# Kernel tuning notes

Measured on AMD Instinct MI355X. Metric: run time of the kernel, lower is better.

Reference implementation:

```python
import jax, jax.numpy as jnp
import numpy as np

N_LEVELS = 16
N_FEATS = 2
LOG2_T = 19
BASE_RES = 16.0
FINEST_RES = 512.0
N_POINTS = 1_000_000
HASH_MASK = np.uint32((1 << LOG2_T) - 1)
PRIME1 = np.uint32(2654435761)  # second spatial-hash prime (first is 1)


def setup_inputs() -> dict:
    key = jax.random.key(0)
    k1, k2 = jax.random.split(key)
    x = jax.random.uniform(k1, (N_POINTS, 2), dtype=jnp.float32)
    # nn.init.uniform_(w, -1e-4, 1e-4) per level, stacked: [L, T, F]
    embeddings = (jax.random.uniform(k2, (N_LEVELS, 2 ** LOG2_T, N_FEATS), dtype=jnp.float32) * 2.0 - 1.0) * 1e-4
    return {"x": x, "embeddings": embeddings}


def reference(x, embeddings):
    L = N_LEVELS
    n = x.shape[0]
    # per-level resolutions: floor(base * b**i)
    b = np.exp((np.log(FINEST_RES) - np.log(BASE_RES)) / (L - 1))
    res = np.floor(BASE_RES * b ** np.arange(L)).astype(np.float32)  # [L]
    res_j = jnp.asarray(res)

    pixels = x[None, :, :] * res_j[:, None, None]           # [L, n, 2]
    top_left = jnp.floor(pixels).astype(jnp.int32)          # [L, n, 2]
    offsets = jnp.array([[0, 0], [1, 0], [0, 1], [1, 1]], dtype=jnp.int32)
    box = top_left[:, :, None, :] + offsets[None, None]     # [L, n, 4, 2]
    box = jnp.clip(box, 0, res_j[:, None, None, None].astype(jnp.int32))

    # spatial hash: (c0*1 ^ c1*prime) & mask, with uint32 wraparound like torch int32
    c = box.astype(jnp.uint32)
    addr = ((c[..., 0] * np.uint32(1)) ^ (c[..., 1] * PRIME1)) & HASH_MASK  # [L, n, 4]
    addr = addr.astype(jnp.int32)

    # gather per-level corner features: [L, n, 4, F]
    feats = jax.vmap(lambda table, idx: table[idx])(embeddings, addr)

    # bilinear interpolation
    w = pixels - jnp.floor(pixels)                          # [L, n, 2]
    w0 = w[..., 0:1]
    w1 = w[..., 1:2]
    f0, f1, f2, f3 = feats[:, :, 0], feats[:, :, 1], feats[:, :, 2], feats[:, :, 3]
    f = (f0 * (1 - w0) + f1 * w0) * (1 - w1) + (f2 * (1 - w0) + f3 * w0) * w1  # [L, n, F]

    # concat levels along feature dim -> [n, L*F]
    return jnp.transpose(f, (1, 0, 2)).reshape(n, L * N_FEATS)
```

## Files before the change

### kernel.cpp

```cpp
#include <hip/hip_runtime.h>
#include <hip/hip_fp16.h>
#include <cmath>

#define NLVL 16
#define TSIZE (1u << 19)
#define HMASK ((1u << 19) - 1u)
#define PRIME1 2654435761u
#define FSCALE 1024.0f
#define FINV   (1.0f/1024.0f)

typedef float f32x4 __attribute__((ext_vector_type(4)));
typedef unsigned int       u32;
typedef unsigned long long u64;

struct Params {
    float rf[NLVL];
    int   ri[NLVL];
    int   base[NLVL];
    int   stride[NLVL];
};

__device__ __forceinline__ float2 h2f(u32 u) {
    __half2 h; __builtin_memcpy(&h, &u, 4);
    return __half22float2(h);
}

__global__ __launch_bounds__(256) void build_dense_h(
    const float2* __restrict__ emb, u32* __restrict__ dense, Params p)
{
    const int l  = blockIdx.y;
    const int cy = blockIdx.x;
    const int ri = p.ri[l];
    if (cy > ri) return;
    const unsigned hy = (unsigned)cy * PRIME1;
    const u64* tab = (const u64*)(emb + (size_t)l * TSIZE);
    u32* drow = dense + p.base[l] + (size_t)cy * p.stride[l];
    for (int cx = threadIdx.x; cx <= ri; cx += 256) {
        u64 raw = __builtin_nontemporal_load(tab + (((unsigned)cx ^ hy) & HMASK));
        float2 v; __builtin_memcpy(&v, &raw, 8);
        const u32 h0 = (u32)__half_as_ushort(__float2half_rn(v.x * FSCALE));
        const u32 h1 = (u32)__half_as_ushort(__float2half_rn(v.y * FSCALE));
        drow[cx] = h0 | (h1 << 16);
    }
}

__global__ __launch_bounds__(256) void hash_embed_h(
    const float2* __restrict__ x,
    const u32*    __restrict__ dense,
    float*        __restrict__ out,
    Params p, int n)
{
    __shared__ float lds[NLVL * 512];
    const int tid = threadIdx.x;
    const int i = blockIdx.x * 256 + tid;
    float2 xy = make_float2(0.f, 0.f);
    if (i < n) xy = x[i];

    #pragma unroll
    for (int half = 0; half < 2; ++half) {
        u32 q0x[8], q0y[8], q1x[8], q1y[8];
        float w0v[8], w1v[8];
        int edge[8];
        #pragma unroll
        for (int j = 0; j < 8; ++j) {
            const int l = half * 8 + j;
            const float rf = p.rf[l];
            const int ri = p.ri[l];
            const float px = xy.x * rf, py = xy.y * rf;
            const float fx = floorf(px), fy = floorf(py);
            w0v[j] = px - fx;
            w1v[j] = py - fy;
            const int tx = (int)fx, ty = (int)fy;
            const int cx0 = min(tx, ri);
            const int cy0 = min(ty, ri);
            const int cy1 = min(ty + 1, ri);
            edge[j] = (cx0 == ri);
            const u32* tab = dense + p.base[l];
            uint2 a, b;
            __builtin_memcpy(&a, tab + cy0 * p.stride[l] + cx0, 8);
            __builtin_memcpy(&b, tab + cy1 * p.stride[l] + cx0, 8);
            q0x[j] = a.x; q0y[j] = a.y; q1x[j] = b.x; q1y[j] = b.y;
        }
        #pragma unroll
        for (int j = 0; j < 8; ++j) {
            const int l = half * 8 + j;
            const float w0 = w0v[j], w1 = w1v[j];
            const float u0 = 1.f - w0, u1 = 1.f - w1;
            const float2 e00 = h2f(q0x[j]);
            const float2 e01 = h2f(edge[j] ? q0x[j] : q0y[j]);
            const float2 e10 = h2f(q1x[j]);
            const float2 e11 = h2f(edge[j] ? q1x[j] : q1y[j]);
            const float g0 = ((e00.x*u0 + e01.x*w0)*u1 + (e10.x*u0 + e11.x*w0)*w1) * FINV;
            const float g1 = ((e00.y*u0 + e01.y*w0)*u1 + (e10.y*u0 + e11.y*w0)*w1) * FINV;
            const int idx = l * 512 + ((2 * tid) ^ ((l & 15) << 1));
            lds[idx]     = g0;
            lds[idx + 1] = g1;
        }
    }
    __syncthreads();

    const long long total = (long long)n * 32;
    const long long base  = (long long)blockIdx.x * 8192;
    #pragma unroll
    for (int it = 0; it < 8; ++it) {
        const int k = (it * 256 + tid) * 4;
        if (base + k < total) {
            const int p2 = k >> 5;
            const int l0 = (k & 31) >> 1;
            const int s0 = l0 * 512       + ((2 * p2) ^ ((l0 & 15) << 1));
            const int s1 = (l0 + 1) * 512 + ((2 * p2) ^ (((l0 + 1) & 15) << 1));
            f32x4 v;
            v.x = lds[s0]; v.y = lds[s0 + 1];
            v.z = lds[s1]; v.w = lds[s1 + 1];
            __builtin_nontemporal_store(v, (f32x4*)(out + base + k));
        }
    }
}

__global__ __launch_bounds__(256) void hash_embed_direct(
    const float2* __restrict__ x,
    const float2* __restrict__ emb,
    float* __restrict__ out,
    Params p, int n)
{
    __shared__ float2 lds[NLVL * 256];
    const int tid = threadIdx.x;
    const int i = blockIdx.x * 256 + tid;
    float2 xy = make_float2(0.f, 0.f);
    if (i < n) xy = x[i];

    #pragma unroll
    for (int half = 0; half < 2; ++half) {
        float2 f[32];
        float w0v[8], w1v[8];
        #pragma unroll
        for (int j = 0; j < 8; ++j) {
            const int l = half * 8 + j;
            const float rf = p.rf[l];
            const int ri = p.ri[l];
            const float px = xy.x * rf, py = xy.y * rf;
            const float fx = floorf(px), fy = floorf(py);
            w0v[j] = px - fx;
            w1v[j] = py - fy;
            const int tx = (int)fx, ty = (int)fy;
            const unsigned cx0 = (unsigned)min(tx, ri);
            const unsigned cy0 = (unsigned)min(ty, ri);
            const unsigned cx1 = (unsigned)min(tx + 1, ri);
            const unsigned cy1 = (unsigned)min(ty + 1, ri);
            const unsigned hy0 = cy0 * PRIME1;
            const unsigned hy1 = cy1 * PRIME1;
            const float2* tab = emb + (size_t)l * TSIZE;
            f[j*4+0] = tab[(cx0 ^ hy0) & HMASK];
            f[j*4+1] = tab[(cx1 ^ hy0) & HMASK];
            f[j*4+2] = tab[(cx0 ^ hy1) & HMASK];
            f[j*4+3] = tab[(cx1 ^ hy1) & HMASK];
        }
        #pragma unroll
        for (int j = 0; j < 8; ++j) {
            const int l = half * 8 + j;
            const float w0 = w0v[j], w1 = w1v[j];
            const float u0 = 1.f - w0, u1 = 1.f - w1;
            const float2 f0 = f[j*4+0], f1 = f[j*4+1], f2 = f[j*4+2], f3 = f[j*4+3];
            const float g0 = (f0.x*u0 + f1.x*w0)*u1 + (f2.x*u0 + f3.x*w0)*w1;
            const float g1 = (f0.y*u0 + f1.y*w0)*u1 + (f2.y*u0 + f3.y*w0)*w1;
            lds[l * 256 + tid] = make_float2(g0, g1);
        }
    }
    __syncthreads();

    const float* lf = (const float*)lds;
    const long long total = (long long)n * 32;
    const long long base = (long long)blockIdx.x * 8192;
    #pragma unroll
    for (int it = 0; it < 8; ++it) {
        const int k = (it * 256 + tid) * 4;
        if (base + k < total) {
            const int p2 = k >> 5;
            const int l0 = (k & 31) >> 1;
            float4 v;
            v.x = lf[(l0 * 256 + p2) * 2 + 0];
            v.y = lf[(l0 * 256 + p2) * 2 + 1];
            v.z = lf[((l0 + 1) * 256 + p2) * 2 + 0];
            v.w = lf[((l0 + 1) * 256 + p2) * 2 + 1];
            *(float4*)(out + base + k) = v;
        }
    }
}

extern "C" void kernel_launch(void* const* d_in, const int* in_sizes, int n_in,
                              void* d_out, int out_size, void* d_ws, size_t ws_size,
                              hipStream_t stream) {
    const float2* x = (const float2*)d_in[0];
    const float2* emb = (const float2*)d_in[1];
    float* out = (float*)d_out;
    const int n = in_sizes[0] / 2;

    Params p;
    int off = 0;
    const double b = std::exp((std::log(512.0) - std::log(16.0)) / 15.0);
    for (int l = 0; l < NLVL; ++l) {
        const double r = std::floor(16.0 * std::pow(b, (double)l));
        p.rf[l] = (float)r;
        p.ri[l] = (int)r;
        p.stride[l] = p.ri[l] + 2;
        p.base[l] = off;
        off += (p.ri[l] + 1) * (p.ri[l] + 2);
    }
    const size_t need = (size_t)off * sizeof(u32);

    const int grid = (n + 255) / 256;
    if (ws_size >= need) {
        build_dense_h<<<dim3(513, 16), 256, 0, stream>>>(emb, (u32*)d_ws, p);
        hash_embed_h<<<grid, 256, 0, stream>>>(x, (const u32*)d_ws, out, p, n);
    } else {
        hash_embed_direct<<<grid, 256, 0, stream>>>(x, emb, out, p, n);
    }
}
```

Before: 240.2 us.

## Drop LDS transpose and issue all 16 level gathers before interpolating

Replaces the shared-memory staging and coalesced block-wide output write with direct per-thread 128-byte row stores of 16B vectors, and removes the __syncthreads. All 16 levels' dense-table loads are now issued up front instead of in two halves of 8, which raises memory-level parallelism at the cost of more registers. The risk is that per-thread strided stores (each lane writing its own 128B row) coalesce worse than the previous contiguous nontemporal stores, and the higher register use may reduce occupancy.

```diff
diff --git a/kernel.cpp b/kernel.cpp
--- a/kernel.cpp
+++ b/kernel.cpp
@@ -44,75 +44,61 @@
     }
 }
 
-__global__ __launch_bounds__(256) void hash_embed_h(
+__global__ __launch_bounds__(256) void hash_embed_flat(
     const float2* __restrict__ x,
     const u32*    __restrict__ dense,
     float*        __restrict__ out,
     Params p, int n)
 {
-    __shared__ float lds[NLVL * 512];
-    const int tid = threadIdx.x;
-    const int i = blockIdx.x * 256 + tid;
-    float2 xy = make_float2(0.f, 0.f);
-    if (i < n) xy = x[i];
+    const int i = blockIdx.x * 256 + threadIdx.x;
+    if (i >= n) return;
+    u64 raw = __builtin_nontemporal_load((const u64*)(x + i));
+    float2 xy; __builtin_memcpy(&xy, &raw, 8);
+    float* dst = out + (size_t)i * 32;
+
+    u32 q0x[NLVL], q0y[NLVL], q1x[NLVL], q1y[NLVL];
+    float w0v[NLVL], w1v[NLVL];
+    int edge[NLVL];
+
+    #pragma unroll
+    for (int l = 0; l < NLVL; ++l) {
+        const float rf = p.rf[l];
+        const int ri = p.ri[l];
+        const float px = xy.x * rf, py = xy.y * rf;
+        const float fx = floorf(px), fy = floorf(py);
+        w0v[l] = px - fx;
+        w1v[l] = py - fy;
+        const int tx = (int)fx, ty = (int)fy;
+        const int cx0 = min(tx, ri);
+        const int cy0 = min(ty, ri);
+        const int cy1 = min(ty + 1, ri);
+        edge[l] = (cx0 == ri);
+        const u32* tab = dense + p.base[l];
+        uint2 a, b;
+        __builtin_memcpy(&a, tab + cy0 * p.stride[l] + cx0, 8);
+        __builtin_memcpy(&b, tab + cy1 * p.stride[l] + cx0, 8);
+        q0x[l] = a.x; q0y[l] = a.y; q1x[l] = b.x; q1y[l] = b.y;
+    }
 
     #pragma unroll
     for (int half = 0; half < 2; ++half) {
-        u32 q0x[8], q0y[8], q1x[8], q1y[8];
-        float w0v[8], w1v[8];
-        int edge[8];
+        float g[16];
         #pragma unroll
         for (int j = 0; j < 8; ++j) {
             const int l = half * 8 + j;
-            const float rf = p.rf[l];
-            const int ri = p.ri[l];
-            const float px = xy.x * rf, py = xy.y * rf;
-            const float fx = floorf(px), fy = floorf(py);
-            w0v[j] = px - fx;
-            w1v[j] = py - fy;
-            const int tx = (int)fx, ty = (int)fy;
-            const int cx0 = min(tx, ri);
-            const int cy0 = min(ty, ri);
-            const int cy1 = min(ty + 1, ri);
-            edge[j] = (cx0 == ri);
-            const u32* tab = dense + p.base[l];
-            uint2 a, b;
-            __builtin_memcpy(&a, tab + cy0 * p.stride[l] + cx0, 8);
-            __builtin_memcpy(&b, tab + cy1 * p.stride[l] + cx0, 8);
-            q0x[j] = a.x; q0y[j] = a.y; q1x[j] = b.x; q1y[j] = b.y;
-        }
-        #pragma unroll
-        for (int j = 0; j < 8; ++j) {
-            const int l = half * 8 + j;
-            const float w0 = w0v[j], w1 = w1v[j];
+            const float w0 = w0v[l], w1 = w1v[l];
             const float u0 = 1.f - w0, u1 = 1.f - w1;
-            const float2 e00 = h2f(q0x[j]);
-            const float2 e01 = h2f(edge[j] ? q0x[j] : q0y[j]);
-            const float2 e10 = h2f(q1x[j]);
-            const float2 e11 = h2f(edge[j] ? q1x[j] : q1y[j]);
-            const float g0 = ((e00.x*u0 + e01.x*w0)*u1 + (e10.x*u0 + e11.x*w0)*w1) * FINV;
-            const float g1 = ((e00.y*u0 + e01.y*w0)*u1 + (e10.y*u0 + e11.y*w0)*w1) * FINV;
-            const int idx = l * 512 + ((2 * tid) ^ ((l & 15) << 1));
-            lds[idx]     = g0;
-            lds[idx + 1] = g1;
-        }
-    }
-    __syncthreads();
-
-    const long long total = (long long)n * 32;
-    const long long base  = (long long)blockIdx.x * 8192;
-    #pragma unroll
-    for (int it = 0; it < 8; ++it) {
-        const int k = (it * 256 + tid) * 4;
-        if (base + k < total) {
-            const int p2 = k >> 5;
-            const int l0 = (k & 31) >> 1;
-            const int s0 = l0 * 512       + ((2 * p2) ^ ((l0 & 15) << 1));
-            const int s1 = (l0 + 1) * 512 + ((2 * p2) ^ (((l0 + 1) & 15) << 1));
-            f32x4 v;
-            v.x = lds[s0]; v.y = lds[s0 + 1];
-            v.z = lds[s1]; v.w = lds[s1 + 1];
-            __builtin_nontemporal_store(v, (f32x4*)(out + base + k));
+            const float2 e00 = h2f(q0x[l]);
+            const float2 e01 = h2f(edge[l] ? q0x[l] : q0y[l]);
+            const float2 e10 = h2f(q1x[l]);
+            const float2 e11 = h2f(edge[l] ? q1x[l] : q1y[l]);
+            g[j*2+0] = ((e00.x*u0 + e01.x*w0)*u1 + (e10.x*u0 + e11.x*w0)*w1) * FINV;
+            g[j*2+1] = ((e00.y*u0 + e01.y*w0)*u1 + (e10.y*u0 + e11.y*w0)*w1) * FINV;
+        }
+        #pragma unroll
+        for (int q = 0; q < 4; ++q) {
+            f32x4 v; v.x = g[q*4+0]; v.y = g[q*4+1]; v.z = g[q*4+2]; v.w = g[q*4+3];
+            *(f32x4*)(dst + half * 16 + q * 4) = v;
         }
     }
 }
@@ -211,7 +197,7 @@
     const int grid = (n + 255) / 256;
     if (ws_size >= need) {
         build_dense_h<<<dim3(513, 16), 256, 0, stream>>>(emb, (u32*)d_ws, p);
-        hash_embed_h<<<grid, 256, 0, stream>>>(x, (const u32*)d_ws, out, p, n);
+        hash_embed_flat<<<grid, 256, 0, stream>>>(x, (const u32*)d_ws, out, p, n);
     } else {
         hash_embed_direct<<<grid, 256, 0, stream>>>(x, emb, out, p, n);
     }
```

Result: slower. 293.4 us (+22.1%).
